# Kernel optimization log

Measured on AMD Instinct MI355X. Metric: run time of the kernel, lower is better.

Reference implementation:

```python
import jax, jax.numpy as jnp
import numpy as np

N_QUBITS = 6
N_LAYERS = 8
N_CLASSES = 4
BATCH = 262144
DIM = 2 ** N_QUBITS  # 64


def setup_inputs() -> dict:
    key = jax.random.key(0)
    k1, k2, k3, k4 = jax.random.split(key, 4)
    x = jax.random.normal(k1, (BATCH, DIM), dtype=jnp.float32)
    # TorchLayer default init for StronglyEntanglingLayers weights: U(0, 2*pi)
    weights = jax.random.uniform(k2, (N_LAYERS, N_QUBITS, 3), dtype=jnp.float32,
                                 minval=0.0, maxval=2.0 * np.pi)
    fc_w = jax.random.normal(k3, (N_CLASSES, N_QUBITS), dtype=jnp.float32) * 0.3
    fc_b = jax.random.normal(k4, (N_CLASSES,), dtype=jnp.float32) * 0.1
    return {"x": x, "weights": weights, "fc_w": fc_w, "fc_b": fc_b}


def _rot_mats(weights):
    # PennyLane Rot(phi, theta, omega) = RZ(omega) RY(theta) RZ(phi)
    phi, theta, omega = weights[..., 0], weights[..., 1], weights[..., 2]
    c = jnp.cos(theta / 2)
    s = jnp.sin(theta / 2)
    m00 = jnp.exp(-0.5j * (phi + omega)) * c
    m01 = -jnp.exp(0.5j * (phi - omega)) * s
    m10 = jnp.exp(-0.5j * (phi - omega)) * s
    m11 = jnp.exp(0.5j * (phi + omega)) * c
    # [L, n, 2, 2] complex64
    return jnp.stack([jnp.stack([m00, m01], -1), jnp.stack([m10, m11], -1)], -2).astype(jnp.complex64)


def _apply_1q(state, U, q):
    # state: [B, 2, 2, 2, 2, 2, 2]; apply 2x2 gate U on qubit axis q+1
    ax = q + 1
    s = jnp.moveaxis(state, ax, -1)
    s = jnp.einsum('ij,...j->...i', U, s)
    return jnp.moveaxis(s, -1, ax)


def _cnot(state, c, t):
    # flip target qubit t on the control==1 slice of qubit c
    axc = c + 1
    s0 = jax.lax.index_in_dim(state, 0, axis=axc, keepdims=False)
    s1 = jax.lax.index_in_dim(state, 1, axis=axc, keepdims=False)
    t_ax = t + 1 if t < c else t  # target axis after removing control axis
    s1 = jnp.flip(s1, axis=t_ax)
    return jnp.stack([s0, s1], axis=axc)


def _pauli_z_signs():
    # qubit 0 is the most significant bit of the basis-state index
    bits = (jnp.arange(DIM)[:, None] >> jnp.arange(N_QUBITS - 1, -1, -1)[None, :]) & 1
    return (1 - 2 * bits).astype(jnp.float32)  # [DIM, N_QUBITS]


def reference(x, weights, fc_w, fc_b):
    B = x.shape[0]
    # F.normalize(p=2) + AmplitudeEmbedding(normalize=True) -> single L2 normalize
    xn = x / jnp.maximum(jnp.linalg.norm(x, axis=1, keepdims=True), 1e-12)
    state = xn.astype(jnp.complex64).reshape((B,) + (2,) * N_QUBITS)
    U = _rot_mats(weights)  # [L, n, 2, 2]
    for l in range(N_LAYERS):
        for q in range(N_QUBITS):
            state = _apply_1q(state, U[l, q], q)
        r = (l % (N_QUBITS - 1)) + 1  # StronglyEntanglingLayers default ranges
        for q in range(N_QUBITS):
            state = _cnot(state, q, (q + r) % N_QUBITS)
    probs = (state.real ** 2 + state.imag ** 2).reshape(B, DIM)
    expvals = probs @ _pauli_z_signs()  # [B, n] <Z_i>
    return expvals @ fc_w.T + fc_b
```

## Files before the change

kernel.cpp:

```cpp
#include <hip/hip_runtime.h>

#define NQ 6
#define DIM 64
#define NL 8

#define WP  72

typedef __attribute__((ext_vector_type(4))) float    floatx4;
typedef __attribute__((ext_vector_type(4))) _Float16 half4v;

__global__ __launch_bounds__(64) void qnn_prep(
    const float* __restrict__ wts,
    const float* __restrict__ fc_w,
    void* __restrict__ ws)
{
    __shared__ float gc[48][4];
    const int n   = threadIdx.x;
    const int col = blockIdx.x;

    if (n < 48) {
        float phi = wts[n*3+0], th = wts[n*3+1], om = wts[n*3+2];
        float ch = cosf(0.5f*th), sh = sinf(0.5f*th);
        float p  = 0.5f*(phi+om), m  = 0.5f*(phi-om);
        gc[n][0] = cosf(p)*ch;
        gc[n][1] = sinf(p)*ch;
        gc[n][2] = cosf(m)*sh;
        gc[n][3] = sinf(m)*sh;
    }
    __syncthreads();

    float ar = (n == col) ? 1.0f : 0.0f;
    float ai = 0.0f;

    #pragma unroll
    for (int l = 0; l < NL; ++l) {
        #pragma unroll
        for (int q = 0; q < NQ; ++q) {
            const int g     = l*NQ + q;
            const int shift = 5 - q;
            const int mask  = 1 << shift;
            const int b     = (n >> shift) & 1;
            const float cpch = gc[g][0];
            const float spch = gc[g][1];
            const float cmsh = gc[g][2];
            const float smsh = gc[g][3];
            const float pr = __shfl_xor(ar, mask, 64);
            const float pi = __shfl_xor(ai, mask, 64);
            const float udr = cpch;
            const float udi = b ?  spch : -spch;
            const float uor = b ?  cmsh : -cmsh;
            const float uoi = -smsh;
            const float nr = udr*ar - udi*ai + uor*pr - uoi*pi;
            const float ni = udr*ai + udi*ar + uor*pi + uoi*pr;
            ar = nr; ai = ni;
        }
        const int r = (l % (NQ - 1)) + 1;
        #pragma unroll
        for (int q = 0; q < NQ; ++q) {
            const int t     = (q + r) % NQ;
            const int cmask = 1 << (5 - q);
            const int tmask = 1 << (5 - t);
            const float pr = __shfl_xor(ar, tmask, 64);
            const float pi = __shfl_xor(ai, tmask, 64);
            const bool ctrl = (n & cmask) != 0;
            ar = ctrl ? pr : ar;
            ai = ctrl ? pi : ai;
        }
    }

    _Float16* Wf = (_Float16*)ws;
    Wf[n*WP + col]      = (_Float16)ar;
    Wf[(64+n)*WP + col] = (_Float16)ai;

    if (col == 0) {
        const int cp = n & 15;
        const int qd = n >> 4;
        half4v* Mo = (half4v*)((char*)ws + 128*WP*2);
        #pragma unroll
        for (int c2 = 0; c2 < 4; ++c2) {
            half4v h4;
            #pragma unroll
            for (int j = 0; j < 4; ++j) {
                const int i = c2*16 + qd*4 + j;
                float v = 0.f;
                if (cp < 4) {
                    #pragma unroll
                    for (int q = 0; q < NQ; ++q) {
                        const float sgn = 1.0f - 2.0f*(float)((i >> (5-q)) & 1);
                        v = fmaf(sgn, fc_w[cp*NQ + q], v);
                    }
                } else if (cp == 4) {
                    v = 1.0f;
                }
                h4[j] = (_Float16)v;
            }
            Mo[c2*64 + n] = h4;
        }
    }
}

__global__ __launch_bounds__(256, 4) void qnn_main(
    const float* __restrict__ x,
    const float* __restrict__ fc_b,
    const void* __restrict__ wsv,
    float* __restrict__ out)
{
    __shared__ __align__(16) _Float16 Ws[128*WP];

    const int tid  = threadIdx.x;
    const int lane = tid & 63;
    const int w    = tid >> 6;
    const int l15  = lane & 15;
    const int quad = lane >> 4;
    const size_t gw = (size_t)blockIdx.x*4 + w;

    float4 xr[2][4];
    #pragma unroll
    for (int t = 0; t < 2; ++t) {
        const float* xp = x + (gw*32 + (size_t)t*16 + l15)*DIM + quad*4;
        #pragma unroll
        for (int kc = 0; kc < 4; ++kc)
            xr[t][kc] = *(const float4*)(xp + kc*16);
    }

    {
        const floatx4* wg = (const floatx4*)wsv;
        floatx4* wl = (floatx4*)Ws;
        #pragma unroll
        for (int i = 0; i < 5; ++i) {
            const int idx = tid + i*256;
            if (idx < 128*WP*2/16) wl[idx] = wg[idx];
        }
    }

    const half4v* Mg = (const half4v*)((const char*)wsv + 128*WP*2);
    half4v a2[4];
    #pragma unroll
    for (int c2 = 0; c2 < 4; ++c2) a2[c2] = Mg[c2*64 + lane];
    const float b0 = fc_b[0], b1 = fc_b[1], b2 = fc_b[2], b3 = fc_b[3];

    __syncthreads();

    #pragma unroll
    for (int t = 0; t < 2; ++t) {
        half4v xf[4];
        #pragma unroll
        for (int kc = 0; kc < 4; ++kc) {
            const float4 u = xr[t][kc];
            half4v h;
            h[0] = (_Float16)u.x; h[1] = (_Float16)u.y;
            h[2] = (_Float16)u.z; h[3] = (_Float16)u.w;
            xf[kc] = h;
        }

        floatx4 acc[8];
        #pragma unroll
        for (int mt = 0; mt < 8; ++mt) acc[mt] = (floatx4){0.f, 0.f, 0.f, 0.f};

        #pragma unroll
        for (int kc = 0; kc < 4; ++kc) {
            #pragma unroll
            for (int mt = 0; mt < 8; ++mt) {
                const half4v wf = *(const half4v*)
                    &Ws[(mt*16 + l15)*WP + kc*16 + quad*4];
                acc[mt] = __builtin_amdgcn_mfma_f32_16x16x16f16(
                    wf, xf[kc], acc[mt], 0, 0, 0);
            }
        }

        floatx4 d2 = (floatx4){0.f, 0.f, 0.f, 0.f};
        #pragma unroll
        for (int c2 = 0; c2 < 4; ++c2) {
            half4v pb;
            #pragma unroll
            for (int r = 0; r < 4; ++r) {
                const float re = acc[c2][r];
                const float im = acc[c2 + 4][r];
                pb[r] = (_Float16)fmaf(re, re, im*im);
            }
            d2 = __builtin_amdgcn_mfma_f32_16x16x16f16(a2[c2], pb, d2, 0, 0, 0);
        }
        const float ssv = __shfl_xor(d2[0], 16, 64);
        if (quad == 0) {
            const float inv = 1.0f / ssv;
            float4 o;
            o.x = fmaf(d2[0], inv, b0);
            o.y = fmaf(d2[1], inv, b1);
            o.z = fmaf(d2[2], inv, b2);
            o.w = fmaf(d2[3], inv, b3);
            *(float4*)(out + (gw*32 + (size_t)t*16 + l15)*4) = o;
        }
    }
}

extern "C" void kernel_launch(void* const* d_in, const int* in_sizes, int n_in,
                              void* d_out, int out_size, void* d_ws, size_t ws_size,
                              hipStream_t stream) {
    const float* x    = (const float*)d_in[0];
    const float* wts  = (const float*)d_in[1];
    const float* fc_w = (const float*)d_in[2];
    const float* fc_b = (const float*)d_in[3];
    float* out = (float*)d_out;

    qnn_prep<<<DIM, DIM, 0, stream>>>(wts, fc_w, d_ws);
    qnn_main<<<2048, 256, 0, stream>>>(x, fc_b, d_ws, out);
}
```

Baseline: 108.9 us.

## Use 16x16x32 f16 MFMA with register-resident weights instead of LDS staging

Switches the main GEMM from 16x16x16 to the gfx950 16x16x32 f16 MFMA, halving the MFMA count per tile. The weight fragments are now loaded straight from global memory (L2-cached workspace) into registers, which removes the shared-memory staging and the block barrier. x loads are regrouped into 8-wide chunks to match the new K layout. This raises register pressure, and occupancy is lowered to 3 blocks per CU in exchange.

```diff
diff --git a/kernel.cpp b/kernel.cpp
--- a/kernel.cpp
+++ b/kernel.cpp
@@ -8,6 +8,7 @@
 
 typedef __attribute__((ext_vector_type(4))) float    floatx4;
 typedef __attribute__((ext_vector_type(4))) _Float16 half4v;
+typedef __attribute__((ext_vector_type(8))) _Float16 half8v;
 
 __global__ __launch_bounds__(64) void qnn_prep(
     const float* __restrict__ wts,
@@ -99,14 +100,12 @@
     }
 }
 
-__global__ __launch_bounds__(256, 4) void qnn_main(
+__global__ __launch_bounds__(256, 3) void qnn_main(
     const float* __restrict__ x,
     const float* __restrict__ fc_b,
     const void* __restrict__ wsv,
     float* __restrict__ out)
 {
-    __shared__ __align__(16) _Float16 Ws[128*WP];
-
     const int tid  = threadIdx.x;
     const int lane = tid & 63;
     const int w    = tid >> 6;
@@ -114,24 +113,24 @@
     const int quad = lane >> 4;
     const size_t gw = (size_t)blockIdx.x*4 + w;
 
-    float4 xr[2][4];
+    float4 xr[2][2][2];
     #pragma unroll
     for (int t = 0; t < 2; ++t) {
-        const float* xp = x + (gw*32 + (size_t)t*16 + l15)*DIM + quad*4;
-        #pragma unroll
-        for (int kc = 0; kc < 4; ++kc)
-            xr[t][kc] = *(const float4*)(xp + kc*16);
-    }
-
-    {
-        const floatx4* wg = (const floatx4*)wsv;
-        floatx4* wl = (floatx4*)Ws;
-        #pragma unroll
-        for (int i = 0; i < 5; ++i) {
-            const int idx = tid + i*256;
-            if (idx < 128*WP*2/16) wl[idx] = wg[idx];
-        }
-    }
+        const float* xp = x + (gw*32 + (size_t)t*16 + l15)*DIM + quad*8;
+        #pragma unroll
+        for (int kk = 0; kk < 2; ++kk) {
+            xr[t][kk][0] = *(const float4*)(xp + kk*32);
+            xr[t][kk][1] = *(const float4*)(xp + kk*32 + 4);
+        }
+    }
+
+    const _Float16* Wf = (const _Float16*)wsv;
+    half8v wfr[2][8];
+    #pragma unroll
+    for (int kk = 0; kk < 2; ++kk)
+        #pragma unroll
+        for (int mt = 0; mt < 8; ++mt)
+            wfr[kk][mt] = *(const half8v*)(Wf + (mt*16 + l15)*WP + kk*32 + quad*8);
 
     const half4v* Mg = (const half4v*)((const char*)wsv + 128*WP*2);
     half4v a2[4];
@@ -139,34 +138,30 @@
     for (int c2 = 0; c2 < 4; ++c2) a2[c2] = Mg[c2*64 + lane];
     const float b0 = fc_b[0], b1 = fc_b[1], b2 = fc_b[2], b3 = fc_b[3];
 
-    __syncthreads();
-
     #pragma unroll
     for (int t = 0; t < 2; ++t) {
-        half4v xf[4];
-        #pragma unroll
-        for (int kc = 0; kc < 4; ++kc) {
-            const float4 u = xr[t][kc];
-            half4v h;
-            h[0] = (_Float16)u.x; h[1] = (_Float16)u.y;
-            h[2] = (_Float16)u.z; h[3] = (_Float16)u.w;
-            xf[kc] = h;
+        half8v xf[2];
+        #pragma unroll
+        for (int kk = 0; kk < 2; ++kk) {
+            const float4 u0 = xr[t][kk][0];
+            const float4 u1 = xr[t][kk][1];
+            half8v h;
+            h[0] = (_Float16)u0.x; h[1] = (_Float16)u0.y;
+            h[2] = (_Float16)u0.z; h[3] = (_Float16)u0.w;
+            h[4] = (_Float16)u1.x; h[5] = (_Float16)u1.y;
+            h[6] = (_Float16)u1.z; h[7] = (_Float16)u1.w;
+            xf[kk] = h;
         }
 
         floatx4 acc[8];
         #pragma unroll
         for (int mt = 0; mt < 8; ++mt) acc[mt] = (floatx4){0.f, 0.f, 0.f, 0.f};
-
-        #pragma unroll
-        for (int kc = 0; kc < 4; ++kc) {
+        #pragma unroll
+        for (int kk = 0; kk < 2; ++kk)
             #pragma unroll
-            for (int mt = 0; mt < 8; ++mt) {
-                const half4v wf = *(const half4v*)
-                    &Ws[(mt*16 + l15)*WP + kc*16 + quad*4];
-                acc[mt] = __builtin_amdgcn_mfma_f32_16x16x16f16(
-                    wf, xf[kc], acc[mt], 0, 0, 0);
-            }
-        }
+            for (int mt = 0; mt < 8; ++mt)
+                acc[mt] = __builtin_amdgcn_mfma_f32_16x16x32_f16(
+                    wfr[kk][mt], xf[kk], acc[mt], 0, 0, 0);
 
         floatx4 d2 = (floatx4){0.f, 0.f, 0.f, 0.f};
         #pragma unroll
```

Measured after the change: 107.3 us. Within noise of the previous version (-1.5%).
